# Kernel tuning notes

Hardware: AMD Instinct MI355X
Metric: run time of the kernel (lower is better)

## Reference

```python
import jax, jax.numpy as jnp
import numpy as np

B, S, D, H = 2, 2048, 1024, 16
HD = D // H          # 64
NREF = HD // 2       # 32 Householder reflections
BLOCK = 128          # flex_attention block granularity
ROPE_BASE = 10000.0


def setup_inputs() -> dict:
    key = jax.random.key(0)
    ks = jax.random.split(key, 12)
    x = jax.random.normal(ks[0], (B, S, D), jnp.float32)
    # block-causal block mask (flex_attention block_mask analogue)
    nb = S // BLOCK
    bm = jnp.tril(jnp.ones((nb, nb), bool))
    mask = jnp.repeat(jnp.repeat(bm, BLOCK, axis=0), BLOCK, axis=1)  # [S,S]
    s = lambda fan: fan ** -0.5
    vs = jax.random.normal(ks[1], (NREF, HD), jnp.float32) * 0.02
    w_qkv = jax.random.normal(ks[2], (D, 3 * D), jnp.float32) * s(D)
    w_out = jax.random.normal(ks[3], (D, D), jnp.float32) * s(D)
    w_gate = jax.random.normal(ks[4], (D, D), jnp.float32) * s(D)
    b_gate = jnp.zeros((D,), jnp.float32)
    w_mlp_gate = jax.random.normal(ks[5], (D, 8 * D), jnp.float32) * s(D)
    b_mlp_gate = jnp.zeros((8 * D,), jnp.float32)
    w_mlp_out = jax.random.normal(ks[6], (4 * D, D), jnp.float32) * s(4 * D)
    b_mlp_out = jnp.zeros((D,), jnp.float32)
    return dict(x=x, mask=mask, grid_size=S, vs=vs, w_qkv=w_qkv, w_out=w_out,
                w_gate=w_gate, b_gate=b_gate, w_mlp_gate=w_mlp_gate,
                b_mlp_gate=b_mlp_gate, w_mlp_out=w_mlp_out, b_mlp_out=b_mlp_out)


def rmsnorm(x):
    return x * jax.lax.rsqrt(jnp.mean(x * x, axis=-1, keepdims=True) + 1e-6)


def householder_matrix(vs):
    # Q = prod_i (I - 2 v_i v_i^T / |v_i|^2), applied sequentially as in torch loop
    def body(Q, v):
        vn = jnp.sum(v * v) + 1e-8
        return Q - (2.0 / vn) * jnp.outer(v, v @ Q), None
    Q0 = jnp.eye(HD, dtype=vs.dtype)
    Q, _ = jax.lax.scan(body, Q0, vs)
    return Q


def rope_tables(seq_len, dtype):
    inv_freq = 1.0 / (ROPE_BASE ** (jnp.arange(0, HD, 2, dtype=jnp.float32) / HD))
    ang = jnp.arange(seq_len, dtype=jnp.float32)[:, None] * inv_freq  # [S, HD/2]
    ang = jnp.concatenate([ang, ang], axis=-1)                        # [S, HD]
    return jnp.cos(ang).astype(dtype), jnp.sin(ang).astype(dtype)


def rotate_half(x):
    x1, x2 = jnp.split(x, 2, axis=-1)
    return jnp.concatenate([-x2, x1], axis=-1)


def reference(x, mask, grid_size, vs, w_qkv, w_out, w_gate, b_gate,
              w_mlp_gate, b_mlp_gate, w_mlp_out, b_mlp_out):
    del grid_size  # positions derived from sequence length
    resid = x
    h = rmsnorm(x)
    qkv = h @ w_qkv                                # [B,S,3D]
    q, k, v = jnp.split(qkv, 3, axis=-1)
    to_heads = lambda t: t.reshape(B, S, H, HD).transpose(0, 2, 1, 3)  # [B,H,S,hd]
    q, k, v = to_heads(q), to_heads(k), to_heads(v)

    # RnRoPE: inverse Householder rotation, rope, forward Householder rotation
    Q = householder_matrix(vs)                     # [hd,hd]
    q = q @ Q.T
    k = k @ Q.T
    cos, sin = rope_tables(S, x.dtype)             # [S,hd]
    cos = cos[None, None]; sin = sin[None, None]
    q = q * cos + rotate_half(q) * sin
    k = k * cos + rotate_half(k) * sin
    q = q @ Q
    k = k @ Q

    # block-sparse attention (mask realized as boolean [S,S])
    scores = jnp.einsum('bhqd,bhkd->bhqk', q, k) / jnp.sqrt(jnp.asarray(HD, x.dtype))
    scores = jnp.where(mask[None, None], scores, jnp.asarray(-1e30, x.dtype))
    attn = jnp.einsum('bhqk,bhkd->bhqd', jax.nn.softmax(scores, axis=-1), v)
    attn = attn.transpose(0, 2, 1, 3).reshape(B, S, D)
    attn = attn @ w_out

    gate = jax.nn.sigmoid(attn @ w_gate + b_gate)
    x = resid + attn * gate

    resid = x
    gv = rmsnorm(x) @ w_mlp_gate + b_mlp_gate      # [B,S,8D]
    g, val = jnp.split(gv, 2, axis=-1)
    x = resid + (val * jax.nn.gelu(g, approximate=False)) @ w_mlp_out + b_mlp_out
    return x
```

## Files before the change

### kernel.cpp

```cpp
#include <hip/hip_runtime.h>
#include <hip/hip_bf16.h>
#include <math.h>

#define BT 2
#define SEQ 2048
#define DIM 1024
#define NH 16
#define HD 64
#define NTOK (BT*SEQ)

typedef __attribute__((ext_vector_type(4))) float floatx4;
typedef __attribute__((ext_vector_type(8))) short shortx8;
typedef __attribute__((ext_vector_type(4))) short shortx4;

#define GLL16(gp, lp) __builtin_amdgcn_global_load_lds( \
    (const __attribute__((address_space(1))) unsigned int*)(const void*)(gp), \
    (__attribute__((address_space(3))) unsigned int*)(void*)(lp), 16, 0, 0)

__device__ __forceinline__ float bf2f(unsigned short u) {
    unsigned int x = ((unsigned int)u) << 16;
    return __builtin_bit_cast(float, x);
}
__device__ __forceinline__ unsigned short f2bf(float f) {
    unsigned int x = __builtin_bit_cast(unsigned int, f);
    unsigned int lsb = (x >> 16) & 1u;
    x += 0x7fffu + lsb;
    return (unsigned short)(x >> 16);
}
__device__ __forceinline__ float ldin_f(const void* p, size_t i, int isbf) {
    return isbf ? bf2f(((const unsigned short*)p)[i]) : ((const float*)p)[i];
}

__global__ void detect_kernel(const unsigned short* __restrict__ x, int* __restrict__ flag) {
    __shared__ int cnt;
    if (threadIdx.x == 0) cnt = 0;
    __syncthreads();
    unsigned short u = x[(size_t)threadIdx.x * 2];
    int e = (u >> 7) & 0xFF;
    if (e >= 100 && e <= 140) atomicAdd(&cnt, 1);
    __syncthreads();
    if (threadIdx.x == 0) *flag = (cnt >= 192) ? 1 : 0;
}

__global__ void transpose_any(const void* __restrict__ in,
                              unsigned short* __restrict__ out, int R, int C,
                              const int* __restrict__ flagp) {
    int isbf = *flagp;
    __shared__ unsigned short tile[32][33];
    int c0 = blockIdx.x * 32, r0 = blockIdx.y * 32;
    int tx = threadIdx.x, ty = threadIdx.y;
#pragma unroll
    for (int i = 0; i < 4; i++) {
        size_t idx = (size_t)(r0 + ty + i * 8) * C + c0 + tx;
        tile[ty + i * 8][tx] = isbf ? ((const unsigned short*)in)[idx]
                                    : f2bf(((const float*)in)[idx]);
    }
    __syncthreads();
#pragma unroll
    for (int i = 0; i < 4; i++)
        out[(size_t)(c0 + ty + i * 8) * R + r0 + tx] = tile[tx][ty + i * 8];
}

__global__ __launch_bounds__(64) void householder_kernel(const void* __restrict__ vs,
                                                         float* __restrict__ Qg,
                                                         const int* __restrict__ flagp) {
    int isbf = *flagp;
    __shared__ float vsh[64];
    int j = threadIdx.x;
    float Qc[64];
#pragma unroll
    for (int i = 0; i < 64; i++) Qc[i] = (i == j) ? 1.f : 0.f;
    for (int r = 0; r < 32; r++) {
        vsh[j] = ldin_f(vs, r * 64 + j, isbf);
        __syncthreads();
        float va[64];
#pragma unroll
        for (int i = 0; i < 64; i++) va[i] = vsh[i];
        float vn0 = 0.f, vn1 = 0.f, vn2 = 0.f, vn3 = 0.f;
        float t0 = 0.f, t1 = 0.f, t2 = 0.f, t3 = 0.f;
#pragma unroll
        for (int i = 0; i < 16; i++) {
            vn0 += va[4 * i + 0] * va[4 * i + 0];
            vn1 += va[4 * i + 1] * va[4 * i + 1];
            vn2 += va[4 * i + 2] * va[4 * i + 2];
            vn3 += va[4 * i + 3] * va[4 * i + 3];
            t0 += va[4 * i + 0] * Qc[4 * i + 0];
            t1 += va[4 * i + 1] * Qc[4 * i + 1];
            t2 += va[4 * i + 2] * Qc[4 * i + 2];
            t3 += va[4 * i + 3] * Qc[4 * i + 3];
        }
        float vn = (vn0 + vn1) + (vn2 + vn3) + 1e-8f;
        float t = (t0 + t1) + (t2 + t3);
        float c = (2.f / vn) * t;
#pragma unroll
        for (int i = 0; i < 64; i++) Qc[i] -= c * va[i];
        __syncthreads();
    }
#pragma unroll
    for (int i = 0; i < 64; i++) Qg[i * 64 + j] = Qc[i];
}

__global__ __launch_bounds__(256) void rotate_wqkv(unsigned short* __restrict__ wT,
                                                   const float* __restrict__ Qg) {
    __shared__ float Qs[64][64];
    __shared__ unsigned short tile[64][128];
    int bid = blockIdx.x;
    int row0 = (bid >> 3) * 64;
    int col0 = (bid & 7) * 128;
    int t = threadIdx.x;
#pragma unroll
    for (int i = 0; i < 16; i++) {
        int idx = i * 256 + t;
        Qs[idx >> 6][idx & 63] = Qg[idx];
    }
#pragma unroll
    for (int i = 0; i < 8; i++) {
        int e = i * 256 + t;
        int r = e >> 5, cg = (e & 31) * 4;
        *(shortx4*)&tile[r][cg] = *(const shortx4*)&wT[(size_t)(row0 + r) * 1024 + col0 + cg];
    }
    __syncthreads();
    int ib = t >> 5;
    int c = (t & 31) * 4;
    float acc[8][4];
#pragma unroll
    for (int rr = 0; rr < 8; rr++)
#pragma unroll
        for (int cx = 0; cx < 4; cx++) acc[rr][cx] = 0.f;
    for (int j = 0; j < 64; j++) {
        float t0 = bf2f(tile[j][c]);
        float t1 = bf2f(tile[j][c + 1]);
        float t2 = bf2f(tile[j][c + 2]);
        float t3 = bf2f(tile[j][c + 3]);
#pragma unroll
        for (int rr = 0; rr < 8; rr++) {
            float qv = Qs[rr * 8 + ib][j];
            acc[rr][0] += qv * t0;
            acc[rr][1] += qv * t1;
            acc[rr][2] += qv * t2;
            acc[rr][3] += qv * t3;
        }
    }
#pragma unroll
    for (int rr = 0; rr < 8; rr++) {
        int i = rr * 8 + ib;
        shortx4 o4;
#pragma unroll
        for (int cx = 0; cx < 4; cx++) o4[cx] = (short)f2bf(acc[rr][cx]);
        *(shortx4*)&wT[(size_t)(row0 + i) * 1024 + col0 + c] = o4;
    }
}

__global__ void rope_table(float* __restrict__ tab) {
    int idx = blockIdx.x * 256 + threadIdx.x;
    int s = idx >> 5, fi = idx & 31;
    float invf = __expf(-(float)fi * (9.210340371976184f / 32.f));
    float ang = (float)s * invf;
    tab[2 * idx]     = cosf(ang);
    tab[2 * idx + 1] = sinf(ang);
}

__global__ __launch_bounds__(256) void rmsnorm2(const void* __restrict__ x,
                                                unsigned short* __restrict__ h,
                                                const int* __restrict__ flagp) {
    int isbf = flagp ? *flagp : 1;
    __shared__ float wred[4];
    int row = blockIdx.x, t = threadIdx.x;
    size_t base = (size_t)row * DIM;
    float v[4];
    float ss = 0.f;
#pragma unroll
    for (int i = 0; i < 4; i++) {
        v[i] = ldin_f(x, base + t + 256 * i, isbf);
        ss += v[i] * v[i];
    }
#pragma unroll
    for (int m = 1; m < 64; m <<= 1) ss += __shfl_xor(ss, m, 64);
    if ((t & 63) == 0) wred[t >> 6] = ss;
    __syncthreads();
    float tot = (wred[0] + wred[1]) + (wred[2] + wred[3]);
    float rs = rsqrtf(tot * (1.f / 1024.f) + 1e-6f);
#pragma unroll
    for (int i = 0; i < 4; i++) h[base + t + 256 * i] = f2bf(v[i] * rs);
}

template<int MODE, int GM, int GN>
__global__ __launch_bounds__(256) void gemm_bt(const unsigned short* __restrict__ A,
                                               const unsigned short* __restrict__ Bt,
                                               void* __restrict__ C,
                                               const void* __restrict__ bias,
                                               const unsigned short* __restrict__ resid,
                                               const void* __restrict__ xin,
                                               const int* __restrict__ flagp,
                                               int M, int N, int K) {
    __shared__ __align__(16) unsigned short As[2][128][64];
    __shared__ __align__(16) unsigned short Bs[2][64][64];
    int isbf = flagp ? *flagp : 1;
    int t0 = (blockIdx.x & 7) * (gridDim.x >> 3) + (blockIdx.x >> 3);
    int nbn = N >> 6;
    constexpr int SB = GM * GN;
    int s0 = t0 / SB, inner = t0 % SB;
    int sbn = nbn / GN;
    int m0 = ((s0 / sbn) * GM + (inner % GM)) * 128;
    int n0 = ((s0 % sbn) * GN + (inner / GM)) * 64;
    int t = threadIdx.x;
    int lane = t & 63;
    int w = t >> 6;
    int wr = (w >> 1) * 64;
    int wc = (w & 1) * 32;
    int lr = lane & 15;
    int kg = lane >> 4;
    int l8 = lane >> 3, s8 = lane & 7;
    int segswz = (s8 ^ l8) * 8;
    int cs0 = ((kg)     ^ (lr & 7)) * 8;
    int cs1 = ((4 + kg) ^ (lr & 7)) * 8;

    floatx4 acc[4][2];
#pragma unroll
    for (int i = 0; i < 4; i++)
#pragma unroll
        for (int j = 0; j < 2; j++) acc[i][j] = (floatx4){0.f, 0.f, 0.f, 0.f};

    int rbase = w * 8 + l8;
    const unsigned short* aP0 = A + (size_t)(m0 + rbase +  0) * K + segswz;
    const unsigned short* aP1 = A + (size_t)(m0 + rbase + 32) * K + segswz;
    const unsigned short* aP2 = A + (size_t)(m0 + rbase + 64) * K + segswz;
    const unsigned short* aP3 = A + (size_t)(m0 + rbase + 96) * K + segswz;
    const unsigned short* bP0 = Bt + (size_t)(n0 + rbase +  0) * K + segswz;
    const unsigned short* bP1 = Bt + (size_t)(n0 + rbase + 32) * K + segswz;

    auto STAGE = [&](int s, int B) {
        int off = s * 64;
        GLL16(aP0 + off, &As[B][w * 8 +  0][0]);
        GLL16(aP1 + off, &As[B][w * 8 + 32][0]);
        GLL16(aP2 + off, &As[B][w * 8 + 64][0]);
        GLL16(aP3 + off, &As[B][w * 8 + 96][0]);
        GLL16(bP0 + off, &Bs[B][w * 8 +  0][0]);
        GLL16(bP1 + off, &Bs[B][w * 8 + 32][0]);
    };
    auto MM = [&](int B) {
        shortx8 af[4][2], bf[2][2];
#pragma unroll
        for (int i = 0; i < 4; i++) {
            af[i][0] = *(const shortx8*)&As[B][wr + i * 16 + lr][cs0];
            af[i][1] = *(const shortx8*)&As[B][wr + i * 16 + lr][cs1];
        }
#pragma unroll
        for (int j = 0; j < 2; j++) {
            bf[j][0] = *(const shortx8*)&Bs[B][wc + j * 16 + lr][cs0];
            bf[j][1] = *(const shortx8*)&Bs[B][wc + j * 16 + lr][cs1];
        }
#pragma unroll
        for (int i = 0; i < 4; i++)
#pragma unroll
            for (int j = 0; j < 2; j++) {
                acc[i][j] = __builtin_amdgcn_mfma_f32_16x16x32_bf16(af[i][0], bf[j][0], acc[i][j], 0, 0, 0);
                acc[i][j] = __builtin_amdgcn_mfma_f32_16x16x32_bf16(af[i][1], bf[j][1], acc[i][j], 0, 0, 0);
            }
    };

    int NS = K >> 6;
    STAGE(0, 0);
    __syncthreads();
    for (int s = 0; s < NS; s += 2) {
        if (s + 1 < NS) STAGE(s + 1, 1);
        MM(0);
        __syncthreads();
        if (s + 1 < NS) {
            if (s + 2 < NS) STAGE(s + 2, 0);
            MM(1);
            __syncthreads();
        }
    }
#pragma unroll
    for (int i = 0; i < 4; i++) {
#pragma unroll
        for (int j = 0; j < 2; j++) {
            int col = n0 + wc + j * 16 + lr;
            int rb = m0 + wr + i * 16 + kg * 4;
            float bv = bias ? ldin_f(bias, col, isbf) : 0.f;
#pragma unroll
            for (int r = 0; r < 4; r++) {
                float val = acc[i][j][r] + bv;
                size_t oidx = (size_t)(rb + r) * N + col;
                if constexpr (MODE == 0) {
                    ((unsigned short*)C)[oidx] = f2bf(val);
                } else if constexpr (MODE == 1) {
                    ((float*)C)[oidx] = val + bf2f(resid[oidx]);
                } else {
                    float a = bf2f(resid[oidx]);
                    float sg = 1.f / (1.f + __expf(-val));
                    ((unsigned short*)C)[oidx] = f2bf(ldin_f(xin, oidx, isbf) + a * sg);
                }
            }
        }
    }
}

__global__ __launch_bounds__(256) void gemm_glu(const unsigned short* __restrict__ A,
                                                const unsigned short* __restrict__ Bt,
                                                unsigned short* __restrict__ act,
                                                const void* __restrict__ bias,
                                                const int* __restrict__ flagp) {
    __shared__ __align__(16) unsigned short As[2][128][64];
    __shared__ __align__(16) unsigned short Bg[2][64][64];
    __shared__ __align__(16) unsigned short Bv[2][64][64];
    const int K = 1024;
    int isbf = *flagp;
    int t0 = (blockIdx.x & 7) * (gridDim.x >> 3) + (blockIdx.x >> 3);
    int s0 = t0 >> 6, inner = t0 & 63;
    int m0 = ((s0 >> 3) * 8 + (inner & 7)) * 128;
    int n0 = ((s0 & 7) * 8 + (inner >> 3)) * 64;
    int t = threadIdx.x;
    int lane = t & 63;
    int w = t >> 6;
    int wr = (w >> 1) * 64;
    int wc = (w & 1) * 32;
    int lr = lane & 15;
    int kg = lane >> 4;
    int l8 = lane >> 3, s8 = lane & 7;
    int segswz = (s8 ^ l8) * 8;
    int cs0 = ((kg)     ^ (lr & 7)) * 8;
    int cs1 = ((4 + kg) ^ (lr & 7)) * 8;

    floatx4 ag[4][2], av[4][2];
#pragma unroll
    for (int i = 0; i < 4; i++)
#pragma unroll
        for (int j = 0; j < 2; j++) {
            ag[i][j] = (floatx4){0.f, 0.f, 0.f, 0.f};
            av[i][j] = (floatx4){0.f, 0.f, 0.f, 0.f};
        }

    int rbase = w * 8 + l8;
    const unsigned short* aP0 = A + (size_t)(m0 + rbase +  0) * K + segswz;
    const unsigned short* aP1 = A + (size_t)(m0 + rbase + 32) * K + segswz;
    const unsigned short* aP2 = A + (size_t)(m0 + rbase + 64) * K + segswz;
    const unsigned short* aP3 = A + (size_t)(m0 + rbase + 96) * K + segswz;
    const unsigned short* gP0 = Bt + (size_t)(n0 + rbase +  0) * K + segswz;
    const unsigned short* gP1 = Bt + (size_t)(n0 + rbase + 32) * K + segswz;
    const unsigned short* vP0 = Bt + (size_t)(4096 + n0 + rbase +  0) * K + segswz;
    const unsigned short* vP1 = Bt + (size_t)(4096 + n0 + rbase + 32) * K + segswz;

    auto STAGE = [&](int s, int B) {
        int off = s * 64;
        GLL16(aP0 + off, &As[B][w * 8 +  0][0]);
        GLL16(aP1 + off, &As[B][w * 8 + 32][0]);
        GLL16(aP2 + off, &As[B][w * 8 + 64][0]);
        GLL16(aP3 + off, &As[B][w * 8 + 96][0]);
        GLL16(gP0 + off, &Bg[B][w * 8 +  0][0]);
        GLL16(gP1 + off, &Bg[B][w * 8 + 32][0]);
        GLL16(vP0 + off, &Bv[B][w * 8 +  0][0]);
        GLL16(vP1 + off, &Bv[B][w * 8 + 32][0]);
    };
    auto MM = [&](int B) {
        shortx8 af[4][2], gf[2][2], vf[2][2];
#pragma unroll
        for (int i = 0; i < 4; i++) {
            af[i][0] = *(const shortx8*)&As[B][wr + i * 16 + lr][cs0];
            af[i][1] = *(const shortx8*)&As[B][wr + i * 16 + lr][cs1];
        }
#pragma unroll
        for (int j = 0; j < 2; j++) {
            gf[j][0] = *(const shortx8*)&Bg[B][wc + j * 16 + lr][cs0];
            gf[j][1] = *(const shortx8*)&Bg[B][wc + j * 16 + lr][cs1];
            vf[j][0] = *(const shortx8*)&Bv[B][wc + j * 16 + lr][cs0];
            vf[j][1] = *(const shortx8*)&Bv[B][wc + j * 16 + lr][cs1];
        }
#pragma unroll
        for (int i = 0; i < 4; i++)
#pragma unroll
            for (int j = 0; j < 2; j++) {
                ag[i][j] = __builtin_amdgcn_mfma_f32_16x16x32_bf16(af[i][0], gf[j][0], ag[i][j], 0, 0, 0);
                ag[i][j] = __builtin_amdgcn_mfma_f32_16x16x32_bf16(af[i][1], gf[j][1], ag[i][j], 0, 0, 0);
                av[i][j] = __builtin_amdgcn_mfma_f32_16x16x32_bf16(af[i][0], vf[j][0], av[i][j], 0, 0, 0);
                av[i][j] = __builtin_amdgcn_mfma_f32_16x16x32_bf16(af[i][1], vf[j][1], av[i][j], 0, 0, 0);
            }
    };

    const int NS = K >> 6;
    STAGE(0, 0);
    __syncthreads();
    for (int s = 0; s < NS; s += 2) {
        if (s + 1 < NS) STAGE(s + 1, 1);
        MM(0);
        __syncthreads();
        if (s + 1 < NS) {
            if (s + 2 < NS) STAGE(s + 2, 0);
            MM(1);
            __syncthreads();
        }
    }
#pragma unroll
    for (int i = 0; i < 4; i++) {
#pragma unroll
        for (int j = 0; j < 2; j++) {
            int col = n0 + wc + j * 16 + lr;
            int rb = m0 + wr + i * 16 + kg * 4;
            float bgv = ldin_f(bias, col, isbf);
            float bvv = ldin_f(bias, 4096 + col, isbf);
#pragma unroll
            for (int r = 0; r < 4; r++) {
                float g = ag[i][j][r] + bgv;
                float v = av[i][j][r] + bvv;
                float ge = 0.5f * g * (1.f + erff(g * 0.70710678118f));
                act[(size_t)(rb + r) * 4096 + col] = f2bf(v * ge);
            }
        }
    }
}

__global__ __launch_bounds__(256) void qk_rope3(const unsigned short* __restrict__ qkv,
                                                const float* __restrict__ tab,
                                                unsigned short* __restrict__ q_r,
                                                unsigned short* __restrict__ k_r) {
    int tid = blockIdx.x * 256 + threadIdx.x;
    int c = tid & 3;
    int h = (tid >> 2) & 15;
    int ts = tid >> 6;
    int s = ts & 2047, b = ts >> 11;
    int d0 = c * 8;
    const unsigned short* base = qkv + (size_t)ts * 3072 + h * 64;
    shortx8 qlo = *(const shortx8*)(base + d0);
    shortx8 qhi = *(const shortx8*)(base + d0 + 32);
    shortx8 klo = *(const shortx8*)(base + 1024 + d0);
    shortx8 khi = *(const shortx8*)(base + 1024 + d0 + 32);
    const float* tp = tab + (size_t)s * 64 + d0 * 2;
    shortx8 oql, oqh, okl, okh;
#pragma unroll
    for (int i = 0; i < 8; i++) {
        float cv = tp[2 * i], sv = tp[2 * i + 1];
        float ql = bf2f((unsigned short)qlo[i]), qh = bf2f((unsigned short)qhi[i]);
        float kl = bf2f((unsigned short)klo[i]), kh = bf2f((unsigned short)khi[i]);
        oql[i] = (short)f2bf(ql * cv - qh * sv);
        oqh[i] = (short)f2bf(qh * cv + ql * sv);
        okl[i] = (short)f2bf(kl * cv - kh * sv);
        okh[i] = (short)f2bf(kh * cv + kl * sv);
    }
    size_t o = ((size_t)(b * NH + h) * SEQ + s) * HD + d0;
    *(shortx8*)(q_r + o)      = oql;
    *(shortx8*)(q_r + o + 32) = oqh;
    *(shortx8*)(k_r + o)      = okl;
    *(shortx8*)(k_r + o + 32) = okh;
}

__global__ __launch_bounds__(512) void attn_mfma(const unsigned short* __restrict__ q_r,
                                                 const unsigned short* __restrict__ k_r,
                                                 const unsigned short* __restrict__ qkv,
                                                 unsigned short* __restrict__ attn) {
    __shared__ __align__(16) unsigned short Ks[64][72];
    __shared__ __align__(16) unsigned short Vt[64 * 72];
    __shared__ __align__(16) unsigned short Ps[8][16][72];
    int bid = blockIdx.x;
    int qblk = 15 - (bid & 15);
    int bh = bid >> 4;
    int b = bh >> 4, h = bh & 15;
    size_t bh_off = (size_t)bh * SEQ * HD;
    int tid = threadIdx.x;
    int wv = tid >> 6, lane = tid & 63;
    int l16 = lane & 15, quad = lane >> 4;
    int q0 = qblk * 128 + wv * 16;

    const unsigned short* qrow = q_r + bh_off + (size_t)(q0 + l16) * HD + quad * 8;
    shortx8 aq0 = *(const shortx8*)(qrow);
    shortx8 aq1 = *(const shortx8*)(qrow + 32);

    floatx4 o[4];
#pragma unroll
    for (int nt = 0; nt < 4; nt++) o[nt] = (floatx4){0.f, 0.f, 0.f, 0.f};
    float m_run = -1e30f, l_run = 0.f;

    int nk = (qblk + 1) * 128;
    int skey = tid >> 3;
    int sd0 = (tid & 7) * 8;
    const unsigned short* kbase = k_r + bh_off + (size_t)skey * HD + sd0;
    const unsigned short* vbase = qkv + ((size_t)(b * SEQ + skey)) * 3072 + 2048 + h * 64 + sd0;
    int vco = (((skey >> 3) ^ (tid & 7)) * 8) + (skey & 7);

    shortx8 kv = *(const shortx8*)kbase;
    shortx8 vvv = *(const shortx8*)vbase;

    for (int k0 = 0; k0 < nk; k0 += 64) {
        __syncthreads();
        *(shortx8*)&Ks[skey][sd0] = kv;
#pragma unroll
        for (int i = 0; i < 8; i++) Vt[(size_t)(sd0 + i) * 72 + vco] = (unsigned short)vvv[i];
        __syncthreads();
        if (k0 + 64 < nk) {
            kv  = *(const shortx8*)(kbase + (size_t)(k0 + 64) * HD);
            vvv = *(const shortx8*)(vbase + (size_t)(k0 + 64) * 3072);
        }

        floatx4 sc[4];
        __builtin_amdgcn_s_setprio(1);
#pragma unroll
        for (int kt = 0; kt < 4; kt++) {
            shortx8 bk0 = *(const shortx8*)&Ks[kt * 16 + l16][quad * 8];
            shortx8 bk1 = *(const shortx8*)&Ks[kt * 16 + l16][32 + quad * 8];
            floatx4 z = (floatx4){0.f, 0.f, 0.f, 0.f};
            z = __builtin_amdgcn_mfma_f32_16x16x32_bf16(bk0, aq0, z, 0, 0, 0);
            z = __builtin_amdgcn_mfma_f32_16x16x32_bf16(bk1, aq1, z, 0, 0, 0);
            sc[kt] = z;
        }
        __builtin_amdgcn_s_setprio(0);
        float sv[16], mx[16];
#pragma unroll
        for (int kt = 0; kt < 4; kt++)
#pragma unroll
            for (int r = 0; r < 4; r++) sv[kt * 4 + r] = sc[kt][r] * 0.125f;
#pragma unroll
        for (int i = 0; i < 16; i++) mx[i] = sv[i];
#pragma unroll
        for (int st = 8; st > 0; st >>= 1)
#pragma unroll
            for (int i = 0; i < 8; i++)
                if (i < st) mx[i] = fmaxf(mx[i], mx[i + st]);
        float mt = mx[0];
        mt = fmaxf(mt, __shfl_xor(mt, 16, 64));
        mt = fmaxf(mt, __shfl_xor(mt, 32, 64));
        float nm = fmaxf(m_run, mt);
        float al = __expf(m_run - nm);
        m_run = nm;
        float p[16];
#pragma unroll
        for (int i = 0; i < 16; i++) p[i] = __expf(sv[i] - nm);
        float sm[8];
#pragma unroll
        for (int i = 0; i < 8; i++) sm[i] = p[i] + p[i + 8];
        float ps = ((sm[0] + sm[1]) + (sm[2] + sm[3])) + ((sm[4] + sm[5]) + (sm[6] + sm[7]));
        ps += __shfl_xor(ps, 16, 64);
        ps += __shfl_xor(ps, 32, 64);
        l_run = l_run * al + ps;
#pragma unroll
        for (int kt = 0; kt < 4; kt++) {
            shortx4 pk;
#pragma unroll
            for (int r = 0; r < 4; r++) pk[r] = (short)f2bf(p[kt * 4 + r]);
            *(shortx4*)&Ps[wv][l16][kt * 16 + quad * 4] = pk;
        }
#pragma unroll
        for (int r = 0; r < 4; r++) {
            float alr = __shfl(al, quad * 4 + r, 64);
            o[0][r] *= alr; o[1][r] *= alr; o[2][r] *= alr; o[3][r] *= alr;
        }
        __builtin_amdgcn_s_setprio(1);
#pragma unroll
        for (int h2 = 0; h2 < 2; h2++) {
            shortx8 ap = *(const shortx8*)&Ps[wv][l16][h2 * 32 + quad * 8];
#pragma unroll
            for (int nt = 0; nt < 4; nt++) {
                int dd = nt * 16 + l16;
                shortx8 bvv = *(const shortx8*)&Vt[(size_t)dd * 72 +
                                                   (((h2 * 4 + quad) ^ ((dd >> 3) & 7)) * 8)];
                o[nt] = __builtin_amdgcn_mfma_f32_16x16x32_bf16(ap, bvv, o[nt], 0, 0, 0);
            }
        }
        __builtin_amdgcn_s_setprio(0);
    }
#pragma unroll
    for (int r = 0; r < 4; r++) {
        float lv = __shfl(l_run, quad * 4 + r, 64);
        float inv_l = 1.f / lv;
        int s = q0 + quad * 4 + r;
        unsigned short* op = attn + ((size_t)(b * SEQ + s)) * DIM + h * 64;
#pragma unroll
        for (int nt = 0; nt < 4; nt++) op[nt * 16 + l16] = f2bf(o[nt][r] * inv_l);
    }
}

extern "C" void kernel_launch(void* const* d_in, const int* in_sizes, int n_in,
                              void* d_out, int out_size, void* d_ws, size_t ws_size,
                              hipStream_t stream) {
    const unsigned short* x        = (const unsigned short*)d_in[0];
    const void* vs       = d_in[3];
    const void* w_qkv    = d_in[4];
    const void* w_out    = d_in[5];
    const void* w_gate   = d_in[6];
    const void* b_gate   = d_in[7];
    const void* w_mlp_g  = d_in[8];
    const void* b_mlp_g  = d_in[9];
    const void* w_mlp_o  = d_in[10];
    const void* b_mlp_o  = d_in[11];
    float* out = (float*)d_out;
    char* ws = (char*)d_ws;

    if (n_in < 12) return;
    if (in_sizes[0] != 4194304 || in_sizes[3] != 2048 || in_sizes[4] != 3145728 ||
        in_sizes[8] != 8388608 || in_sizes[10] != 4194304 || in_sizes[7] != 1024) return;

    const size_t o_T   = 0;
    const size_t o_Qg  = 35651584;
    const size_t o_h   = 35684352;
    const size_t o_B   = 44072960;
    const size_t o_C   = 69238784;
    const size_t o_gv  = 94404608;
    const size_t total = 161513472;
    if (ws_size < total) return;

    unsigned short* wqkvT  = (unsigned short*)(ws + o_T);
    unsigned short* woutT  = (unsigned short*)(ws + o_T + 6291456);
    unsigned short* wgateT = (unsigned short*)(ws + o_T + 8388608);
    unsigned short* wmgT   = (unsigned short*)(ws + o_T + 10485760);
    unsigned short* wmoT   = (unsigned short*)(ws + o_T + 27262976);
    float*          Qg     = (float*)(ws + o_Qg);
    int*            flagp  = (int*)(ws + o_Qg + 16384);
    unsigned short* h      = (unsigned short*)(ws + o_h);
    unsigned short* qkv    = (unsigned short*)(ws + o_B);
    unsigned short* ao     = (unsigned short*)(ws + o_B + 8388608);
    unsigned short* q_rb   = (unsigned short*)(ws + o_C);
    unsigned short* k_rb   = (unsigned short*)(ws + o_C + 8388608);
    unsigned short* attnb  = (unsigned short*)(ws + o_C + 16777216);
    unsigned short* x1     = (unsigned short*)(ws + o_C);
    unsigned short* act    = (unsigned short*)(ws + o_C + 8388608);
    float*          rtab   = (float*)(ws + o_gv);

    detect_kernel<<<1, 256, 0, stream>>>(x, flagp);
    householder_kernel<<<1, 64, 0, stream>>>(vs, Qg, flagp);
    rope_table<<<256, 256, 0, stream>>>(rtab);

    dim3 tb(32, 8);
    transpose_any<<<dim3(3072 / 32, 1024 / 32), tb, 0, stream>>>(w_qkv,   wqkvT, 1024, 3072, flagp);
    transpose_any<<<dim3(1024 / 32, 1024 / 32), tb, 0, stream>>>(w_out,   woutT, 1024, 1024, flagp);
    transpose_any<<<dim3(1024 / 32, 1024 / 32), tb, 0, stream>>>(w_gate,  wgateT, 1024, 1024, flagp);
    transpose_any<<<dim3(8192 / 32, 1024 / 32), tb, 0, stream>>>(w_mlp_g, wmgT, 1024, 8192, flagp);
    transpose_any<<<dim3(1024 / 32, 4096 / 32), tb, 0, stream>>>(w_mlp_o, wmoT, 4096, 1024, flagp);
    rotate_wqkv<<<256, 256, 0, stream>>>(wqkvT, Qg);

    rmsnorm2<<<NTOK, 256, 0, stream>>>(x, h, flagp);
    gemm_bt<0, 4, 8><<<32 * 48, 256, 0, stream>>>(h, wqkvT, qkv, nullptr, nullptr, nullptr, flagp, NTOK, 3072, 1024);
    qk_rope3<<<1024, 256, 0, stream>>>(qkv, rtab, q_rb, k_rb);
    attn_mfma<<<BT * NH * (SEQ / 128), 512, 0, stream>>>(q_rb, k_rb, qkv, attnb);
    gemm_bt<0, 4, 8><<<32 * 16, 256, 0, stream>>>(attnb, woutT, ao, nullptr, nullptr, nullptr, flagp, NTOK, 1024, 1024);
    gemm_bt<2, 4, 8><<<32 * 16, 256, 0, stream>>>(ao, wgateT, x1, b_gate, ao, x, flagp, NTOK, 1024, 1024);
    rmsnorm2<<<NTOK, 256, 0, stream>>>(x1, h, nullptr);
    gemm_glu<<<32 * 64, 256, 0, stream>>>(h, wmgT, act, b_mlp_g, flagp);
    gemm_bt<1, 2, 4><<<32 * 16, 256, 0, stream>>>(act, wmoT, (void*)out, b_mlp_o, x1, nullptr, flagp, NTOK, 1024, 4096);
}
```

Before: 540.7 us.

## Fuse RoPE into attention and merge prep kernels into fewer launches

Removes the separate qk_rope3 pass: attention now reads q and k straight from the qkv buffer and applies the rotary rotation in registers using the cos/sin table. K is rotated per tile, with the partner half loaded as a second vector. Detection and the Householder build are merged into one kernel, and the five weight transposes plus the rope table into a single flat-grid launch. This cuts launch count and the q_r/k_r write and re-read traffic, at the cost of redoing K rotation for every query block and strided K loads.

```diff
diff --git a/kernel.cpp b/kernel.cpp
--- a/kernel.cpp
+++ b/kernel.cpp
@@ -31,24 +31,86 @@
     return isbf ? bf2f(((const unsigned short*)p)[i]) : ((const float*)p)[i];
 }
 
-__global__ void detect_kernel(const unsigned short* __restrict__ x, int* __restrict__ flag) {
+__global__ __launch_bounds__(256) void prep_dh(const unsigned short* __restrict__ x,
+                                               const void* __restrict__ vs,
+                                               float* __restrict__ Qg,
+                                               int* __restrict__ flagp) {
     __shared__ int cnt;
-    if (threadIdx.x == 0) cnt = 0;
+    __shared__ float vsh[64];
+    int t = threadIdx.x;
+    if (t == 0) cnt = 0;
     __syncthreads();
-    unsigned short u = x[(size_t)threadIdx.x * 2];
+    unsigned short u = x[(size_t)t * 2];
     int e = (u >> 7) & 0xFF;
     if (e >= 100 && e <= 140) atomicAdd(&cnt, 1);
     __syncthreads();
-    if (threadIdx.x == 0) *flag = (cnt >= 192) ? 1 : 0;
-}
-
-__global__ void transpose_any(const void* __restrict__ in,
-                              unsigned short* __restrict__ out, int R, int C,
-                              const int* __restrict__ flagp) {
+    int isbf = (cnt >= 192) ? 1 : 0;
+    if (t == 0) *flagp = isbf;
+    int j = t & 63;
+    float Qc[64];
+#pragma unroll
+    for (int i = 0; i < 64; i++) Qc[i] = (i == j) ? 1.f : 0.f;
+    for (int r = 0; r < 32; r++) {
+        if (t < 64) vsh[j] = ldin_f(vs, r * 64 + j, isbf);
+        __syncthreads();
+        if (t < 64) {
+            float va[64];
+#pragma unroll
+            for (int i = 0; i < 64; i++) va[i] = vsh[i];
+            float vn0 = 0.f, vn1 = 0.f, vn2 = 0.f, vn3 = 0.f;
+            float t0 = 0.f, t1 = 0.f, t2 = 0.f, t3 = 0.f;
+#pragma unroll
+            for (int i = 0; i < 16; i++) {
+                vn0 += va[4 * i + 0] * va[4 * i + 0];
+                vn1 += va[4 * i + 1] * va[4 * i + 1];
+                vn2 += va[4 * i + 2] * va[4 * i + 2];
+                vn3 += va[4 * i + 3] * va[4 * i + 3];
+                t0 += va[4 * i + 0] * Qc[4 * i + 0];
+                t1 += va[4 * i + 1] * Qc[4 * i + 1];
+                t2 += va[4 * i + 2] * Qc[4 * i + 2];
+                t3 += va[4 * i + 3] * Qc[4 * i + 3];
+            }
+            float vn = (vn0 + vn1) + (vn2 + vn3) + 1e-8f;
+            float tt = (t0 + t1) + (t2 + t3);
+            float c = (2.f / vn) * tt;
+#pragma unroll
+            for (int i = 0; i < 64; i++) Qc[i] -= c * va[i];
+        }
+        __syncthreads();
+    }
+    if (t < 64)
+#pragma unroll
+        for (int i = 0; i < 64; i++) Qg[i * 64 + j] = Qc[i];
+}
+
+__global__ __launch_bounds__(256) void prep_weights(
+        const void* __restrict__ w_qkv, const void* __restrict__ w_out,
+        const void* __restrict__ w_gate, const void* __restrict__ w_mlp_g,
+        const void* __restrict__ w_mlp_o,
+        unsigned short* __restrict__ wqkvT, unsigned short* __restrict__ woutT,
+        unsigned short* __restrict__ wgateT, unsigned short* __restrict__ wmgT,
+        unsigned short* __restrict__ wmoT,
+        float* __restrict__ rtab, const int* __restrict__ flagp) {
+    int id = blockIdx.x;
+    if (id >= 17408) {
+        int idx = (id - 17408) * 256 + threadIdx.x;
+        int s = idx >> 5, fi = idx & 31;
+        float invf = __expf(-(float)fi * (9.210340371976184f / 32.f));
+        float ang = (float)s * invf;
+        rtab[2 * idx]     = cosf(ang);
+        rtab[2 * idx + 1] = sinf(ang);
+        return;
+    }
+    const void* in; unsigned short* out; int R, C, bx, by;
+    if (id < 3072)       { in = w_qkv;   out = wqkvT;  R = 1024; C = 3072; int i2 = id;         bx = i2 % 96;  by = i2 / 96; }
+    else if (id < 4096)  { in = w_out;   out = woutT;  R = 1024; C = 1024; int i2 = id - 3072;  bx = i2 % 32;  by = i2 / 32; }
+    else if (id < 5120)  { in = w_gate;  out = wgateT; R = 1024; C = 1024; int i2 = id - 4096;  bx = i2 % 32;  by = i2 / 32; }
+    else if (id < 13312) { in = w_mlp_g; out = wmgT;   R = 1024; C = 8192; int i2 = id - 5120;  bx = i2 % 256; by = i2 / 256; }
+    else                 { in = w_mlp_o; out = wmoT;   R = 4096; C = 1024; int i2 = id - 13312; bx = i2 % 32;  by = i2 / 32; }
     int isbf = *flagp;
     __shared__ unsigned short tile[32][33];
-    int c0 = blockIdx.x * 32, r0 = blockIdx.y * 32;
-    int tx = threadIdx.x, ty = threadIdx.y;
+    int c0 = bx * 32, r0 = by * 32;
+    int tx = threadIdx.x & 31, ty = threadIdx.x >> 5;
 #pragma unroll
     for (int i = 0; i < 4; i++) {
         size_t idx = (size_t)(r0 + ty + i * 8) * C + c0 + tx;
@@ -59,45 +121,6 @@
 #pragma unroll
     for (int i = 0; i < 4; i++)
         out[(size_t)(c0 + ty + i * 8) * R + r0 + tx] = tile[tx][ty + i * 8];
-}
-
-__global__ __launch_bounds__(64) void householder_kernel(const void* __restrict__ vs,
-                                                         float* __restrict__ Qg,
-                                                         const int* __restrict__ flagp) {
-    int isbf = *flagp;
-    __shared__ float vsh[64];
-    int j = threadIdx.x;
-    float Qc[64];
-#pragma unroll
-    for (int i = 0; i < 64; i++) Qc[i] = (i == j) ? 1.f : 0.f;
-    for (int r = 0; r < 32; r++) {
-        vsh[j] = ldin_f(vs, r * 64 + j, isbf);
-        __syncthreads();
-        float va[64];
-#pragma unroll
-        for (int i = 0; i < 64; i++) va[i] = vsh[i];
-        float vn0 = 0.f, vn1 = 0.f, vn2 = 0.f, vn3 = 0.f;
-        float t0 = 0.f, t1 = 0.f, t2 = 0.f, t3 = 0.f;
-#pragma unroll
-        for (int i = 0; i < 16; i++) {
-            vn0 += va[4 * i + 0] * va[4 * i + 0];
-            vn1 += va[4 * i + 1] * va[4 * i + 1];
-            vn2 += va[4 * i + 2] * va[4 * i + 2];
-            vn3 += va[4 * i + 3] * va[4 * i + 3];
-            t0 += va[4 * i + 0] * Qc[4 * i + 0];
-            t1 += va[4 * i + 1] * Qc[4 * i + 1];
-            t2 += va[4 * i + 2] * Qc[4 * i + 2];
-            t3 += va[4 * i + 3] * Qc[4 * i + 3];
-        }
-        float vn = (vn0 + vn1) + (vn2 + vn3) + 1e-8f;
-        float t = (t0 + t1) + (t2 + t3);
-        float c = (2.f / vn) * t;
-#pragma unroll
-        for (int i = 0; i < 64; i++) Qc[i] -= c * va[i];
-        __syncthreads();
-    }
-#pragma unroll
-    for (int i = 0; i < 64; i++) Qg[i * 64 + j] = Qc[i];
 }
 
 __global__ __launch_bounds__(256) void rotate_wqkv(unsigned short* __restrict__ wT,
@@ -149,15 +172,6 @@
         for (int cx = 0; cx < 4; cx++) o4[cx] = (short)f2bf(acc[rr][cx]);
         *(shortx4*)&wT[(size_t)(row0 + i) * 1024 + col0 + c] = o4;
     }
-}
-
-__global__ void rope_table(float* __restrict__ tab) {
-    int idx = blockIdx.x * 256 + threadIdx.x;
-    int s = idx >> 5, fi = idx & 31;
-    float invf = __expf(-(float)fi * (9.210340371976184f / 32.f));
-    float ang = (float)s * invf;
-    tab[2 * idx]     = cosf(ang);
-    tab[2 * idx + 1] = sinf(ang);
 }
 
 __global__ __launch_bounds__(256) void rmsnorm2(const void* __restrict__ x,
@@ -410,43 +424,8 @@
     }
 }
 
-__global__ __launch_bounds__(256) void qk_rope3(const unsigned short* __restrict__ qkv,
-                                                const float* __restrict__ tab,
-                                                unsigned short* __restrict__ q_r,
-                                                unsigned short* __restrict__ k_r) {
-    int tid = blockIdx.x * 256 + threadIdx.x;
-    int c = tid & 3;
-    int h = (tid >> 2) & 15;
-    int ts = tid >> 6;
-    int s = ts & 2047, b = ts >> 11;
-    int d0 = c * 8;
-    const unsigned short* base = qkv + (size_t)ts * 3072 + h * 64;
-    shortx8 qlo = *(const shortx8*)(base + d0);
-    shortx8 qhi = *(const shortx8*)(base + d0 + 32);
-    shortx8 klo = *(const shortx8*)(base + 1024 + d0);
-    shortx8 khi = *(const shortx8*)(base + 1024 + d0 + 32);
-    const float* tp = tab + (size_t)s * 64 + d0 * 2;
-    shortx8 oql, oqh, okl, okh;
-#pragma unroll
-    for (int i = 0; i < 8; i++) {
-        float cv = tp[2 * i], sv = tp[2 * i + 1];
-        float ql = bf2f((unsigned short)qlo[i]), qh = bf2f((unsigned short)qhi[i]);
-        float kl = bf2f((unsigned short)klo[i]), kh = bf2f((unsigned short)khi[i]);
-        oql[i] = (short)f2bf(ql * cv - qh * sv);
-        oqh[i] = (short)f2bf(qh * cv + ql * sv);
-        okl[i] = (short)f2bf(kl * cv - kh * sv);
-        okh[i] = (short)f2bf(kh * cv + kl * sv);
-    }
-    size_t o = ((size_t)(b * NH + h) * SEQ + s) * HD + d0;
-    *(shortx8*)(q_r + o)      = oql;
-    *(shortx8*)(q_r + o + 32) = oqh;
-    *(shortx8*)(k_r + o)      = okl;
-    *(shortx8*)(k_r + o + 32) = okh;
-}
-
-__global__ __launch_bounds__(512) void attn_mfma(const unsigned short* __restrict__ q_r,
-                                                 const unsigned short* __restrict__ k_r,
-                                                 const unsigned short* __restrict__ qkv,
+__global__ __launch_bounds__(512) void attn_mfma(const unsigned short* __restrict__ qkv,
+                                                 const float* __restrict__ rtab,
                                                  unsigned short* __restrict__ attn) {
     __shared__ __align__(16) unsigned short Ks[64][72];
     __shared__ __align__(16) unsigned short Vt[64 * 72];
@@ -455,15 +434,25 @@
     int qblk = 15 - (bid & 15);
     int bh = bid >> 4;
     int b = bh >> 4, h = bh & 15;
-    size_t bh_off = (size_t)bh * SEQ * HD;
     int tid = threadIdx.x;
     int wv = tid >> 6, lane = tid & 63;
     int l16 = lane & 15, quad = lane >> 4;
     int q0 = qblk * 128 + wv * 16;
 
-    const unsigned short* qrow = q_r + bh_off + (size_t)(q0 + l16) * HD + quad * 8;
+    const unsigned short* qrow = qkv + ((size_t)(b * SEQ + q0 + l16)) * 3072 + h * 64 + quad * 8;
     shortx8 aq0 = *(const shortx8*)(qrow);
     shortx8 aq1 = *(const shortx8*)(qrow + 32);
+    {
+        const float* qt = rtab + (size_t)(q0 + l16) * 64 + quad * 16;
+#pragma unroll
+        for (int i = 0; i < 8; i++) {
+            float cv = qt[2 * i], sv = qt[2 * i + 1];
+            float ql = bf2f((unsigned short)aq0[i]);
+            float qh = bf2f((unsigned short)aq1[i]);
+            aq0[i] = (short)f2bf(ql * cv - qh * sv);
+            aq1[i] = (short)f2bf(qh * cv + ql * sv);
+        }
+    }
 
     floatx4 o[4];
 #pragma unroll
@@ -473,21 +462,36 @@
     int nk = (qblk + 1) * 128;
     int skey = tid >> 3;
     int sd0 = (tid & 7) * 8;
-    const unsigned short* kbase = k_r + bh_off + (size_t)skey * HD + sd0;
+    int sd0p = sd0 ^ 32;
+    const unsigned short* kb = qkv + ((size_t)(b * SEQ + skey)) * 3072 + 1024 + h * 64;
     const unsigned short* vbase = qkv + ((size_t)(b * SEQ + skey)) * 3072 + 2048 + h * 64 + sd0;
     int vco = (((skey >> 3) ^ (tid & 7)) * 8) + (skey & 7);
-
-    shortx8 kv = *(const shortx8*)kbase;
+    float ksign = (sd0 < 32) ? -1.f : 1.f;
+
+    shortx8 kvA = *(const shortx8*)(kb + sd0);
+    shortx8 kvB = *(const shortx8*)(kb + sd0p);
     shortx8 vvv = *(const shortx8*)vbase;
 
     for (int k0 = 0; k0 < nk; k0 += 64) {
         __syncthreads();
-        *(shortx8*)&Ks[skey][sd0] = kv;
+        {
+            const float* kt = rtab + (size_t)(k0 + skey) * 64 + (sd0 & 31) * 2;
+            shortx8 ko;
+#pragma unroll
+            for (int i = 0; i < 8; i++) {
+                float cv = kt[2 * i], sv = kt[2 * i + 1];
+                float ka = bf2f((unsigned short)kvA[i]);
+                float kp = bf2f((unsigned short)kvB[i]);
+                ko[i] = (short)f2bf(ka * cv + ksign * kp * sv);
+            }
+            *(shortx8*)&Ks[skey][sd0] = ko;
+        }
 #pragma unroll
         for (int i = 0; i < 8; i++) Vt[(size_t)(sd0 + i) * 72 + vco] = (unsigned short)vvv[i];
         __syncthreads();
         if (k0 + 64 < nk) {
-            kv  = *(const shortx8*)(kbase + (size_t)(k0 + 64) * HD);
+            kvA = *(const shortx8*)(kb + (size_t)(k0 + 64) * 3072 + sd0);
+            kvB = *(const shortx8*)(kb + (size_t)(k0 + 64) * 3072 + sd0p);
             vvv = *(const shortx8*)(vbase + (size_t)(k0 + 64) * 3072);
         }
 
@@ -607,29 +611,19 @@
     unsigned short* h      = (unsigned short*)(ws + o_h);
     unsigned short* qkv    = (unsigned short*)(ws + o_B);
     unsigned short* ao     = (unsigned short*)(ws + o_B + 8388608);
-    unsigned short* q_rb   = (unsigned short*)(ws + o_C);
-    unsigned short* k_rb   = (unsigned short*)(ws + o_C + 8388608);
     unsigned short* attnb  = (unsigned short*)(ws + o_C + 16777216);
     unsigned short* x1     = (unsigned short*)(ws + o_C);
     unsigned short* act    = (unsigned short*)(ws + o_C + 8388608);
     float*          rtab   = (float*)(ws + o_gv);
 
-    detect_kernel<<<1, 256, 0, stream>>>(x, flagp);
-    householder_kernel<<<1, 64, 0, stream>>>(vs, Qg, flagp);
-    rope_table<<<256, 256, 0, stream>>>(rtab);
-
-    dim3 tb(32, 8);
-    transpose_any<<<dim3(3072 / 32, 1024 / 32), tb, 0, stream>>>(w_qkv,   wqkvT, 1024, 3072, flagp);
-    transpose_any<<<dim3(1024 / 32, 1024 / 32), tb, 0, stream>>>(w_out,   woutT, 1024, 1024, flagp);
-    transpose_any<<<dim3(1024 / 32, 1024 / 32), tb, 0, stream>>>(w_gate,  wgateT, 1024, 1024, flagp);
-    transpose_any<<<dim3(8192 / 32, 1024 / 32), tb, 0, stream>>>(w_mlp_g, wmgT, 1024, 8192, flagp);
-    transpose_any<<<dim3(1024 / 32, 4096 / 32), tb, 0, stream>>>(w_mlp_o, wmoT, 4096, 1024, flagp);
+    prep_dh<<<1, 256, 0, stream>>>(x, vs, Qg, flagp);
+    prep_weights<<<17664, 256, 0, stream>>>(w_qkv, w_out, w_gate, w_mlp_g, w_mlp_o,
+                                            wqkvT, woutT, wgateT, wmgT, wmoT, rtab, flagp);
     rotate_wqkv<<<256, 256, 0, stream>>>(wqkvT, Qg);
 
     rmsnorm2<<<NTOK, 256, 0, stream>>>(x, h, flagp);
     gemm_bt<0, 4, 8><<<32 * 48, 256, 0, stream>>>(h, wqkvT, qkv, nullptr, nullptr, nullptr, flagp, NTOK, 3072, 1024);
-    qk_rope3<<<1024, 256, 0, stream>>>(qkv, rtab, q_rb, k_rb);
-    attn_mfma<<<BT * NH * (SEQ / 128), 512, 0, stream>>>(q_rb, k_rb, qkv, attnb);
+    attn_mfma<<<BT * NH * (SEQ / 128), 512, 0, stream>>>(qkv, rtab, attnb);
     gemm_bt<0, 4, 8><<<32 * 16, 256, 0, stream>>>(attnb, woutT, ao, nullptr, nullptr, nullptr, flagp, NTOK, 1024, 1024);
     gemm_bt<2, 4, 8><<<32 * 16, 256, 0, stream>>>(ao, wgateT, x1, b_gate, ao, x, flagp, NTOK, 1024, 1024);
     rmsnorm2<<<NTOK, 256, 0, stream>>>(x1, h, nullptr);
```

New measurement: 541.1 us. No clear change (+0.1%).
